# Kernel optimization log

Hardware: AMD Instinct MI355X
Metric: run time of the kernel (lower is better)

Reference implementation:

```python
import jax, jax.numpy as jnp
import numpy as np

N = 50000   # nodes
F = 128     # num_features (per branch)
E = 800000  # edges
G = 16      # graphs in batch
T = 3       # blocks per branch


def setup_inputs() -> dict:
    key = jax.random.key(0)
    ks = jax.random.split(key, 32)
    s = 0.05
    d = {}
    d["x"] = jax.random.normal(ks[0], (N, 2 * F), jnp.float32)
    d["edge_index"] = jax.random.randint(ks[1], (2, E), 0, N)
    d["edge_weight"] = jax.random.uniform(ks[2], (E,), jnp.float32)
    d["batch"] = jnp.sort(jax.random.randint(ks[3], (N,), 0, G))
    d["states"] = jax.random.randint(ks[4], (N,), 0, 2).astype(jnp.float32)

    def w(k, shape):
        return jax.random.normal(k, shape, jnp.float32) * s

    for i, p in enumerate(["p1", "p2"]):
        b = 5 + i * 5
        d[f"{p}_a0"] = w(ks[b], (T,))            # alpha0: Linear(1,1,bias=False) weight per block
        d[f"{p}_a1W"] = w(ks[b + 1], (T, F, F))    # alpha1 weight
        d[f"{p}_a1b"] = w(ks[b + 2], (T, F))       # alpha1 bias
        d[f"{p}_linW"] = w(ks[b + 3], (T, F, F))   # conv.lin weight
        d[f"{p}_linb"] = w(ks[b + 4], (T, F))      # conv.lin bias
    d["beta0_W"] = w(ks[15], (F, F))
    d["beta1_W"] = w(ks[16], (F, F))
    d["beta2_W"] = w(ks[17], (F, 2 * F))
    d["beta2_b"] = w(ks[18], (F,))
    d["gamma0_W"] = w(ks[19], (F, F))
    d["gamma1_W"] = w(ks[20], (F, F))
    d["gamma2_W"] = w(ks[21], (F, F))
    d["gamma3_W"] = w(ks[22], (3 * F // 2, 3 * F))
    d["gamma4_W"] = w(ks[23], (1, 3 * F // 2))
    d["gamma4_b"] = w(ks[24], (1,))
    return d


def _lrelu(v):
    return jax.nn.leaky_relu(v, 0.2)


def _block(x, states, a0, a1W, a1b, linW, linb, src, dst, ew):
    # x = lrelu(alpha1(x + alpha0(states)))
    h = _lrelu((x + states[:, None] * a0) @ a1W.T + a1b)
    # CustomGCNConv: lin then edge-weighted gather/scatter-add (source->target)
    h = h @ linW.T + linb
    msg = ew[:, None] * h[src]  # [E, F]
    return jax.ops.segment_sum(msg, dst, num_segments=x.shape[0])


def reference(x, edge_index, edge_weight, batch, states,
              p1_a0, p1_a1W, p1_a1b, p1_linW, p1_linb,
              p2_a0, p2_a1W, p2_a1b, p2_linW, p2_linb,
              beta0_W, beta1_W, beta2_W, beta2_b,
              gamma0_W, gamma1_W, gamma2_W, gamma3_W, gamma4_W, gamma4_b):
    Fh = x.shape[1] // 2
    x1, x2 = x[:, :Fh], x[:, Fh:]
    s0, s1 = edge_index[0], edge_index[1]
    x1s = jnp.zeros_like(x1)
    x2s = jnp.zeros_like(x2)
    for t in range(T):
        # branch1 uses reversed edges edge_index[[1,0]]
        x1 = _lrelu(_block(x1, states, p1_a0[t], p1_a1W[t], p1_a1b[t],
                           p1_linW[t], p1_linb[t], s1, s0, edge_weight))
        x2 = _lrelu(_block(x2, states, p2_a0[t], p2_a1W[t], p2_a1b[t],
                           p2_linW[t], p2_linb[t], s0, s1, edge_weight))
        x1s = x1s + x1
        x2s = x2s + x2
    xc = _lrelu(jnp.concatenate([x1s @ beta0_W.T, x2s @ beta1_W.T], -1) @ beta2_W.T + beta2_b)
    sel = (states == 1.0)[:, None]
    # per-graph pooled sums broadcast back to nodes (== repeat_interleave since batch is sorted)
    x_s = jax.ops.segment_sum(jnp.where(sel, xc, 0.0), batch, num_segments=G)[batch]
    x_sum = jax.ops.segment_sum(xc, batch, num_segments=G)[batch]
    h = jnp.concatenate([xc @ gamma0_W.T, x_s @ gamma1_W.T, x_sum @ gamma2_W.T], -1)
    h = _lrelu(h @ gamma3_W.T)
    return (h @ gamma4_W.T + gamma4_b).reshape(-1)
```

## Files before the change

kernel.cpp:

```cpp
#include <hip/hip_runtime.h>

typedef short s8v __attribute__((ext_vector_type(8)));
typedef float f32x4 __attribute__((ext_vector_type(4)));

#define LRELU(v) ((v) > 0.f ? (v) : 0.2f * (v))

constexpr int NBK = 391;
constexpr int TILE = 2048;
constexpr int CAP = 4096;

__device__ __forceinline__ float b2f(unsigned short b) {
  return __uint_as_float(((unsigned int)b) << 16);
}
__device__ __forceinline__ unsigned short f2b(float f) {
  unsigned int x = __float_as_uint(f);
  x += 0x7fffu + ((x >> 16) & 1u);
  return (unsigned short)(x >> 16);
}
__device__ __forceinline__ unsigned int pack2(float lo, float hi) {
  return ((unsigned int)f2b(hi) << 16) | (unsigned int)f2b(lo);
}

struct FArgs {
  const unsigned short* X[2];
  const unsigned short* W1[2];
  const float* b1[2];
  const float* a0p[2];
  const float* rowsum[2];
  const unsigned short* W2[2];
  const float* b2[2];
  unsigned short* H[2];
  const float* states;
  int N;
};

__global__ __launch_bounds__(256) void fused_mlp_kernel(FArgs fa)
{
  __shared__ __align__(16) unsigned short Ws[128 * 128];
  __shared__ __align__(16) unsigned short Tp[128 * 128];
  const int d = blockIdx.y;
  const int tid = threadIdx.x;
  const int lane = tid & 63;
  const int w = tid >> 6;
  const int l15 = lane & 15;
  const int g = lane >> 4;
  const int m0 = blockIdx.x * 128;
  const int N = fa.N;

#pragma unroll
  for (int j = 0; j < 8; ++j) {
    int idx = tid + j * 256;
    int o = idx >> 4, c = idx & 15;
    uint4 v = *(const uint4*)(fa.W1[d] + (size_t)o * 128 + c * 8);
    *(uint4*)&Ws[o * 128 + (c ^ (o & 15)) * 8] = v;
  }
  s8v a[2][4];
#pragma unroll
  for (int mf = 0; mf < 2; ++mf) {
    int row = m0 + w * 32 + mf * 16 + l15;
    const unsigned short* ar = fa.X[d] + (size_t)row * 128 + g * 8;
#pragma unroll
    for (int ks = 0; ks < 4; ++ks) {
      s8v t = {};
      if (row < N) t = *(const s8v*)(ar + ks * 32);
      a[mf][ks] = t;
    }
  }
  f32x4 zero4 = {0.f, 0.f, 0.f, 0.f};
  f32x4 acc[2][8];
#pragma unroll
  for (int mf = 0; mf < 2; ++mf)
#pragma unroll
    for (int nf = 0; nf < 8; ++nf) acc[mf][nf] = zero4;
  __syncthreads();
#pragma unroll
  for (int ks = 0; ks < 4; ++ks) {
#pragma unroll
    for (int nf = 0; nf < 8; ++nf) {
      int c = ks * 4 + g;
      s8v b = *(const s8v*)&Ws[(nf * 16 + l15) * 128 + (c ^ l15) * 8];
      acc[0][nf] = __builtin_amdgcn_mfma_f32_16x16x32_bf16(a[0][ks], b, acc[0][nf], 0, 0, 0);
      acc[1][nf] = __builtin_amdgcn_mfma_f32_16x16x32_bf16(a[1][ks], b, acc[1][nf], 0, 0, 0);
    }
  }
  const float a0 = fa.a0p[d][0];
#pragma unroll
  for (int mf = 0; mf < 2; ++mf) {
#pragma unroll
    for (int r = 0; r < 4; ++r) {
      int lrow = w * 32 + mf * 16 + g * 4 + r;
      int row = m0 + lrow;
      float sa = (row < N) ? fa.states[row] * a0 : 0.f;
#pragma unroll
      for (int nf = 0; nf < 8; ++nf) {
        int col = nf * 16 + l15;
        float v = 0.f;
        if (row < N) {
          v = acc[mf][nf][r] + fa.b1[d][col] + sa * fa.rowsum[d][col];
          v = LRELU(v);
        }
        int cch = col >> 3;
        Tp[lrow * 128 + ((cch ^ (lrow & 15)) << 3) + (col & 7)] = f2b(v);
      }
    }
  }
  __syncthreads();
#pragma unroll
  for (int j = 0; j < 8; ++j) {
    int idx = tid + j * 256;
    int o = idx >> 4, c = idx & 15;
    uint4 v = *(const uint4*)(fa.W2[d] + (size_t)o * 128 + c * 8);
    *(uint4*)&Ws[o * 128 + (c ^ (o & 15)) * 8] = v;
  }
  __syncthreads();
#pragma unroll
  for (int mf = 0; mf < 2; ++mf) {
    int lrow = w * 32 + mf * 16 + l15;
#pragma unroll
    for (int ks = 0; ks < 4; ++ks) {
      int c2 = ks * 4 + g;
      a[mf][ks] = *(const s8v*)&Tp[lrow * 128 + ((c2 ^ (lrow & 15)) << 3)];
    }
  }
#pragma unroll
  for (int mf = 0; mf < 2; ++mf)
#pragma unroll
    for (int nf = 0; nf < 8; ++nf) acc[mf][nf] = zero4;
#pragma unroll
  for (int ks = 0; ks < 4; ++ks) {
#pragma unroll
    for (int nf = 0; nf < 8; ++nf) {
      int c = ks * 4 + g;
      s8v b = *(const s8v*)&Ws[(nf * 16 + l15) * 128 + (c ^ l15) * 8];
      acc[0][nf] = __builtin_amdgcn_mfma_f32_16x16x32_bf16(a[0][ks], b, acc[0][nf], 0, 0, 0);
      acc[1][nf] = __builtin_amdgcn_mfma_f32_16x16x32_bf16(a[1][ks], b, acc[1][nf], 0, 0, 0);
    }
  }
#pragma unroll
  for (int mf = 0; mf < 2; ++mf) {
#pragma unroll
    for (int r = 0; r < 4; ++r) {
      int row = m0 + w * 32 + mf * 16 + g * 4 + r;
      if (row >= N) continue;
      unsigned short* crow = fa.H[d] + (size_t)row * 128;
#pragma unroll
      for (int nf = 0; nf < 8; ++nf) {
        int col = nf * 16 + l15;
        crow[col] = f2b(acc[mf][nf][r] + fa.b2[d][col]);
      }
    }
  }
}

struct PBArgs {
  const unsigned short* U[2];
  const unsigned short* Wb[2];
  const unsigned short* Wb2;
  const float* bias;
  unsigned short* XC;
  int N;
};

__global__ __launch_bounds__(256) void fused_beta_kernel(PBArgs pa)
{
  __shared__ __align__(16) unsigned short Ws[128 * 128];
  __shared__ __align__(16) unsigned short Tp[128 * 128];
  const int tid = threadIdx.x;
  const int lane = tid & 63;
  const int w = tid >> 6;
  const int l15 = lane & 15;
  const int g = lane >> 4;
  const int m0 = blockIdx.x * 128;
  const int N = pa.N;
  f32x4 zero4 = {0.f, 0.f, 0.f, 0.f};
  s8v a[2][4];
  f32x4 accf[2][8];
#pragma unroll
  for (int mf = 0; mf < 2; ++mf)
#pragma unroll
    for (int nf = 0; nf < 8; ++nf) accf[mf][nf] = zero4;

  for (int ph = 0; ph < 2; ++ph) {
#pragma unroll
    for (int j = 0; j < 8; ++j) {
      int idx = tid + j * 256;
      int o = idx >> 4, c = idx & 15;
      uint4 v = *(const uint4*)(pa.Wb[ph] + (size_t)o * 128 + c * 8);
      *(uint4*)&Ws[o * 128 + (c ^ (o & 15)) * 8] = v;
    }
#pragma unroll
    for (int mf = 0; mf < 2; ++mf) {
      int row = m0 + w * 32 + mf * 16 + l15;
      const unsigned short* ar = pa.U[ph] + (size_t)row * 128 + g * 8;
#pragma unroll
      for (int ks = 0; ks < 4; ++ks) {
        s8v t = {};
        if (row < N) t = *(const s8v*)(ar + ks * 32);
        a[mf][ks] = t;
      }
    }
    f32x4 acc[2][8];
#pragma unroll
    for (int mf = 0; mf < 2; ++mf)
#pragma unroll
      for (int nf = 0; nf < 8; ++nf) acc[mf][nf] = zero4;
    __syncthreads();
#pragma unroll
    for (int ks = 0; ks < 4; ++ks) {
#pragma unroll
      for (int nf = 0; nf < 8; ++nf) {
        int c = ks * 4 + g;
        s8v b = *(const s8v*)&Ws[(nf * 16 + l15) * 128 + (c ^ l15) * 8];
        acc[0][nf] = __builtin_amdgcn_mfma_f32_16x16x32_bf16(a[0][ks], b, acc[0][nf], 0, 0, 0);
        acc[1][nf] = __builtin_amdgcn_mfma_f32_16x16x32_bf16(a[1][ks], b, acc[1][nf], 0, 0, 0);
      }
    }
    __syncthreads();
#pragma unroll
    for (int mf = 0; mf < 2; ++mf) {
#pragma unroll
      for (int r = 0; r < 4; ++r) {
        int lrow = w * 32 + mf * 16 + g * 4 + r;
        int row = m0 + lrow;
#pragma unroll
        for (int nf = 0; nf < 8; ++nf) {
          int col = nf * 16 + l15;
          float v = (row < N) ? acc[mf][nf][r] : 0.f;
          int cch = col >> 3;
          Tp[lrow * 128 + ((cch ^ (lrow & 15)) << 3) + (col & 7)] = f2b(v);
        }
      }
    }
    __syncthreads();
#pragma unroll
    for (int j = 0; j < 8; ++j) {
      int idx = tid + j * 256;
      int o = idx >> 4, c = idx & 15;
      uint4 v = *(const uint4*)(pa.Wb2 + (size_t)o * 256 + ph * 128 + c * 8);
      *(uint4*)&Ws[o * 128 + (c ^ (o & 15)) * 8] = v;
    }
#pragma unroll
    for (int mf = 0; mf < 2; ++mf) {
      int lrow = w * 32 + mf * 16 + l15;
#pragma unroll
      for (int ks = 0; ks < 4; ++ks) {
        int c2 = ks * 4 + g;
        a[mf][ks] = *(const s8v*)&Tp[lrow * 128 + ((c2 ^ (lrow & 15)) << 3)];
      }
    }
    __syncthreads();
#pragma unroll
    for (int ks = 0; ks < 4; ++ks) {
#pragma unroll
      for (int nf = 0; nf < 8; ++nf) {
        int c = ks * 4 + g;
        s8v b = *(const s8v*)&Ws[(nf * 16 + l15) * 128 + (c ^ l15) * 8];
        accf[0][nf] = __builtin_amdgcn_mfma_f32_16x16x32_bf16(a[0][ks], b, accf[0][nf], 0, 0, 0);
        accf[1][nf] = __builtin_amdgcn_mfma_f32_16x16x32_bf16(a[1][ks], b, accf[1][nf], 0, 0, 0);
      }
    }
    __syncthreads();
  }
#pragma unroll
  for (int mf = 0; mf < 2; ++mf) {
#pragma unroll
    for (int r = 0; r < 4; ++r) {
      int row = m0 + w * 32 + mf * 16 + g * 4 + r;
      if (row >= N) continue;
      unsigned short* crow = pa.XC + (size_t)row * 128;
#pragma unroll
      for (int nf = 0; nf < 8; ++nf) {
        int col = nf * 16 + l15;
        float v = accf[mf][nf][r] + pa.bias[col];
        crow[col] = f2b(LRELU(v));
      }
    }
  }
}

__global__ __launch_bounds__(256) void g3_kernel(
    const unsigned short* __restrict__ xc,
    const unsigned short* __restrict__ A16,
    const unsigned short* __restrict__ B16,
    const int* __restrict__ batch,
    const unsigned short* __restrict__ W0,
    const unsigned short* __restrict__ W3,
    const float* __restrict__ g4W,
    const float* __restrict__ g4b,
    float* __restrict__ out, int N)
{
  constexpr int NF = 12;
  __shared__ __align__(16) unsigned short Ws[192 * 128];
  __shared__ __align__(16) unsigned short Tp[128 * 128];
  const int tid = threadIdx.x;
  const int lane = tid & 63;
  const int w = tid >> 6;
  const int l15 = lane & 15;
  const int g = lane >> 4;
  const int m0 = blockIdx.x * 128;

  f32x4 zero4 = {0.f, 0.f, 0.f, 0.f};
  s8v a[2][4];

#pragma unroll
  for (int j = 0; j < 8; ++j) {
    int idx = tid + j * 256;
    int o = idx >> 4, c = idx & 15;
    uint4 v = *(const uint4*)(W0 + (size_t)o * 128 + c * 8);
    *(uint4*)&Ws[o * 128 + (c ^ (o & 15)) * 8] = v;
  }
#pragma unroll
  for (int mf = 0; mf < 2; ++mf) {
    int row = m0 + w * 32 + mf * 16 + l15;
    const unsigned short* ar = xc + (size_t)row * 128 + g * 8;
#pragma unroll
    for (int ks = 0; ks < 4; ++ks) {
      s8v t = {};
      if (row < N) t = *(const s8v*)(ar + ks * 32);
      a[mf][ks] = t;
    }
  }
  {
    f32x4 acc1[2][8];
#pragma unroll
    for (int mf = 0; mf < 2; ++mf)
#pragma unroll
      for (int nf = 0; nf < 8; ++nf) acc1[mf][nf] = zero4;
    __syncthreads();
#pragma unroll
    for (int ks = 0; ks < 4; ++ks) {
#pragma unroll
      for (int nf = 0; nf < 8; ++nf) {
        int c = ks * 4 + g;
        s8v b = *(const s8v*)&Ws[(nf * 16 + l15) * 128 + (c ^ l15) * 8];
        acc1[0][nf] = __builtin_amdgcn_mfma_f32_16x16x32_bf16(a[0][ks], b, acc1[0][nf], 0, 0, 0);
        acc1[1][nf] = __builtin_amdgcn_mfma_f32_16x16x32_bf16(a[1][ks], b, acc1[1][nf], 0, 0, 0);
      }
    }
#pragma unroll
    for (int mf = 0; mf < 2; ++mf) {
#pragma unroll
      for (int r = 0; r < 4; ++r) {
        int lrow = w * 32 + mf * 16 + g * 4 + r;
        int row = m0 + lrow;
#pragma unroll
        for (int nf = 0; nf < 8; ++nf) {
          int col = nf * 16 + l15;
          float v = (row < N) ? acc1[mf][nf][r] : 0.f;
          int cch = col >> 3;
          Tp[lrow * 128 + ((cch ^ (lrow & 15)) << 3) + (col & 7)] = f2b(v);
        }
      }
    }
  }
  __syncthreads();

  f32x4 acc[2][NF];
#pragma unroll
  for (int mf = 0; mf < 2; ++mf)
#pragma unroll
    for (int nf = 0; nf < NF; ++nf) acc[mf][nf] = zero4;

  int brow[2];
#pragma unroll
  for (int mf = 0; mf < 2; ++mf) {
    int row = m0 + w * 32 + mf * 16 + l15;
    brow[mf] = (row < N) ? batch[row] : 0;
  }

  for (int kk = 0; kk < 384; kk += 128) {
#pragma unroll
    for (int j = 0; j < NF; ++j) {
      int idx = tid + j * 256;
      int o = idx >> 4, c = idx & 15;
      uint4 v = *(const uint4*)(W3 + (size_t)o * 384 + kk + c * 8);
      *(uint4*)&Ws[o * 128 + (c ^ (o & 15)) * 8] = v;
    }
    if (kk == 0) {
#pragma unroll
      for (int mf = 0; mf < 2; ++mf) {
        int lrow = w * 32 + mf * 16 + l15;
#pragma unroll
        for (int ks = 0; ks < 4; ++ks) {
          int c2 = ks * 4 + g;
          a[mf][ks] = *(const s8v*)&Tp[lrow * 128 + ((c2 ^ (lrow & 15)) << 3)];
        }
      }
    } else {
#pragma unroll
      for (int mf = 0; mf < 2; ++mf) {
        int row = m0 + w * 32 + mf * 16 + l15;
        const unsigned short* ar = ((kk == 128) ? A16 : B16) + (size_t)brow[mf] * 128 + g * 8;
#pragma unroll
        for (int ks = 0; ks < 4; ++ks) {
          s8v t = {};
          if (row < N) t = *(const s8v*)(ar + ks * 32);
          a[mf][ks] = t;
        }
      }
    }
    __syncthreads();
#pragma unroll
    for (int ks = 0; ks < 4; ++ks) {
#pragma unroll
      for (int nf = 0; nf < NF; ++nf) {
        int c = ks * 4 + g;
        s8v b = *(const s8v*)&Ws[(nf * 16 + l15) * 128 + (c ^ l15) * 8];
        acc[0][nf] = __builtin_amdgcn_mfma_f32_16x16x32_bf16(a[0][ks], b, acc[0][nf], 0, 0, 0);
        acc[1][nf] = __builtin_amdgcn_mfma_f32_16x16x32_bf16(a[1][ks], b, acc[1][nf], 0, 0, 0);
      }
    }
    if (kk < 256) __syncthreads();
  }

  float w4[NF];
#pragma unroll
  for (int nf = 0; nf < NF; ++nf) w4[nf] = g4W[nf * 16 + l15];
  const float gb = g4b[0];

#pragma unroll
  for (int mf = 0; mf < 2; ++mf) {
#pragma unroll
    for (int r = 0; r < 4; ++r) {
      int row = m0 + w * 32 + mf * 16 + g * 4 + r;
      float dot = 0.f;
#pragma unroll
      for (int nf = 0; nf < NF; ++nf) {
        float v = acc[mf][nf][r];
        v = LRELU(v);
        dot += v * w4[nf];
      }
#pragma unroll
      for (int m = 1; m < 16; m <<= 1) dot += __shfl_xor(dot, m, 16);
      if (l15 == 0 && row < N) out[row] = dot + gb;
    }
  }
}

struct CJobs { const float* s[9]; unsigned short* d[9]; int n[9]; };
__global__ void convert_kernel(CJobs jb) {
  int j = blockIdx.y;
  int idx = (blockIdx.x * 256 + threadIdx.x) * 8;
  if (idx >= jb.n[j]) return;
  const float* s = jb.s[j] + idx;
  float4 p0 = *(const float4*)s;
  float4 p1 = *(const float4*)(s + 4);
  uint4 u;
  u.x = pack2(p0.x, p0.y); u.y = pack2(p0.z, p0.w);
  u.z = pack2(p1.x, p1.y); u.w = pack2(p1.z, p1.w);
  *(uint4*)(jb.d[j] + idx) = u;
}

__global__ void rowsum_kernel(const float* __restrict__ a1,
                              const float* __restrict__ a2, float* __restrict__ rs) {
  int j = blockIdx.x;
  const float* src = (j < 3) ? (a1 + (size_t)j * 16384) : (a2 + (size_t)(j - 3) * 16384);
  int o = threadIdx.x;
  float s = 0.f;
  for (int k = 0; k < 128; ++k) s += src[o * 128 + k];
  rs[j * 128 + o] = s;
}

__global__ void init_kernel(const float* __restrict__ x,
                            unsigned short* __restrict__ x1, unsigned short* __restrict__ x2,
                            int n)
{
  int idx = blockIdx.x * blockDim.x + threadIdx.x;
  int total = n * 16;
  for (; idx < total; idx += gridDim.x * blockDim.x) {
    int r = idx >> 4, c = idx & 15;
    const float* xr = x + (size_t)r * 256 + c * 8;
    float4 p0 = *(const float4*)xr;
    float4 p1 = *(const float4*)(xr + 4);
    uint4 u1;
    u1.x = pack2(p0.x, p0.y); u1.y = pack2(p0.z, p0.w);
    u1.z = pack2(p1.x, p1.y); u1.w = pack2(p1.z, p1.w);
    float4 q0 = *(const float4*)(xr + 128);
    float4 q1 = *(const float4*)(xr + 132);
    uint4 u2;
    u2.x = pack2(q0.x, q0.y); u2.y = pack2(q0.z, q0.w);
    u2.z = pack2(q1.x, q1.y); u2.w = pack2(q1.z, q1.w);
    ((uint4*)(x1 + (size_t)r * 128))[c] = u1;
    ((uint4*)(x2 + (size_t)r * 128))[c] = u2;
  }
}

struct BinArgs {
  const int* s0; const int* s1; const float* ew;
  int* bcur0; int* bcur1;
  unsigned long long* bin0; unsigned long long* bin1;
  int E;
};
__global__ __launch_bounds__(256) void bin_kernel(BinArgs ba)
{
  __shared__ int hist0[NBK], hist1[NBK];
  __shared__ int base0[NBK], base1[NBK];
  const int t = threadIdx.x;
  const int e0 = blockIdx.x * TILE;
  const int e1 = min(e0 + TILE, ba.E);
  for (int i = t; i < NBK; i += 256) { hist0[i] = 0; hist1[i] = 0; }
  __syncthreads();
  for (int e = e0 + t; e < e1; e += 256) {
    atomicAdd(&hist0[ba.s0[e] >> 7], 1);
    atomicAdd(&hist1[ba.s1[e] >> 7], 1);
  }
  __syncthreads();
  for (int i = t; i < NBK; i += 256) {
    int c0 = hist0[i];
    base0[i] = c0 ? atomicAdd(&ba.bcur0[i], c0) : 0;
    int c1 = hist1[i];
    base1[i] = c1 ? atomicAdd(&ba.bcur1[i], c1) : 0;
  }
  __syncthreads();
  for (int i = t; i < NBK; i += 256) { hist0[i] = 0; hist1[i] = 0; }
  __syncthreads();
  for (int e = e0 + t; e < e1; e += 256) {
    int d0 = ba.s0[e], d1 = ba.s1[e];
    unsigned long long wb = (unsigned long long)__float_as_uint(ba.ew[e]) << 32;
    int b0 = d0 >> 7, b1 = d1 >> 7;
    int r0 = base0[b0] + atomicAdd(&hist0[b0], 1);
    if (r0 < CAP)
      ba.bin0[(size_t)b0 * CAP + r0] = wb | (unsigned int)((d0 & 127) << 16) | (unsigned int)d1;
    int r1 = base1[b1] + atomicAdd(&hist1[b1], 1);
    if (r1 < CAP)
      ba.bin1[(size_t)b1 * CAP + r1] = wb | (unsigned int)((d1 & 127) << 16) | (unsigned int)d0;
  }
}

struct BScanArgs { const int* cnt[2]; int* bbase[2]; float* gsel; float* gsum; };
__global__ __launch_bounds__(128) void bscan_kernel(BScanArgs a)
{
  __shared__ int ld[2][NBK];
  int wid = threadIdx.x >> 6, lane = threadIdx.x & 63;
  for (int i = threadIdx.x; i < 2048; i += 128) { a.gsel[i] = 0.f; a.gsum[i] = 0.f; }
  for (int i = lane; i < NBK; i += 64) ld[wid][i] = a.cnt[wid][i];
  __syncthreads();
  if (lane == 0) {
    int acc = 0;
    for (int i = 0; i < NBK; ++i) { int v = ld[wid][i]; ld[wid][i] = acc; acc += v; }
    a.bbase[wid][NBK] = acc;
  }
  __syncthreads();
  for (int i = lane; i < NBK; i += 64) a.bbase[wid][i] = ld[wid][i];
}

struct RArgs {
  const int* bbase[2];
  const unsigned long long* bin[2];
  unsigned int* comb[2];
  int* row[2];
  int n;
};
__global__ __launch_bounds__(256) void reorder_kernel(RArgs ra)
{
  const int d = blockIdx.y;
  const int b = blockIdx.x;
  const unsigned long long* __restrict__ bin = ra.bin[d] + (size_t)b * CAP;
  unsigned int* __restrict__ comb = ra.comb[d];
  int* __restrict__ row = ra.row[d];
  const int nb = b * 128;
  const int ne = min(nb + 128, ra.n);
  const int t = threadIdx.x;
  __shared__ int lcnt[128];
  __shared__ int lcur[128];
  __shared__ int wtot[4];
  if (t < 128) lcnt[t] = 0;
  const int span_beg = ra.bbase[d][b];
  const int span_end = ra.bbase[d][b + 1];
  const int cnt = span_end - span_beg;
  __syncthreads();
  for (int i = t; i < cnt; i += 256) {
    int nl = ((unsigned int)bin[i] >> 16) & 127;
    atomicAdd(&lcnt[nl], 1);
  }
  __syncthreads();
  int lane = t & 63, wv = t >> 6;
  int v = (t < 128) ? lcnt[t] : 0;
  int sc = v;
#pragma unroll
  for (int off = 1; off < 64; off <<= 1) {
    int u = __shfl_up(sc, off, 64);
    if (lane >= off) sc += u;
  }
  if (lane == 63) wtot[wv] = sc;
  __syncthreads();
  int excl = sc - v + ((wv == 1) ? wtot[0] : 0);
  if (t < 128) {
    lcur[t] = excl;
    if (nb + t < ne) row[nb + t] = span_beg + excl;
  }
  if (b == NBK - 1 && t == 0) row[ra.n] = span_end;
  __syncthreads();
  for (int i = t; i < cnt; i += 256) {
    unsigned long long r = bin[i];
    unsigned int lo = (unsigned int)r;
    float w = __uint_as_float((unsigned int)(r >> 32));
    int nl = (lo >> 16) & 127;
    int slot = atomicAdd(&lcur[nl], 1);
    comb[span_beg + slot] = (lo & 0xffffu) | ((unsigned int)f2b(w) << 16);
  }
}

struct GArgs {
  const int* rowstart[2];
  const unsigned int* comb[2];
  const unsigned short* h[2];
  unsigned short* xout[2];
  const unsigned int* add1[2];
  const unsigned int* add2[2];
  int n;
};
__global__ void gather_kernel(GArgs ga)
{
  int quad = blockIdx.x * (blockDim.x >> 6) + (threadIdx.x >> 6);
  int lane = threadIdx.x & 63;
  int sub = lane >> 4;
  int fl = lane & 15;
  long long gnode = (long long)4 * quad + sub;
  bool valid = gnode < 2 * ga.n;
  int dir = (valid && gnode >= ga.n) ? 1 : 0;
  int node = valid ? (int)(gnode - (long long)dir * ga.n) : 0;
  const int* __restrict__ rowstart = ga.rowstart[dir];
  const unsigned int* __restrict__ comb = ga.comb[dir];
  const unsigned int* __restrict__ h = (const unsigned int*)ga.h[dir];
  int beg = rowstart[node], end = rowstart[node + 1];
  if (!valid) end = beg;
  int nch_own = (end - beg + 7) >> 3;
  int m1 = max(nch_own, __shfl_xor(nch_own, 16, 64));
  int nch = max(m1, __shfl_xor(m1, 32, 64));
  float a0 = 0.f, a1 = 0.f, a2 = 0.f, a3 = 0.f;
  float a4 = 0.f, a5 = 0.f, a6 = 0.f, a7 = 0.f;
  for (int ch = 0; ch < nch; ++ch) {
    int p0 = beg + ch * 8;
    unsigned int cc[8];
    uint4 uu[8];
#pragma unroll
    for (int i = 0; i < 8; ++i) {
      int pi = p0 + i;
      cc[i] = (pi < end) ? comb[pi] : 0u;
    }
#pragma unroll
    for (int i = 0; i < 8; ++i)
      uu[i] = *(const uint4*)(h + (size_t)(cc[i] & 0xffffu) * 64 + fl * 4);
#pragma unroll
    for (int i = 0; i < 8; ++i) {
      float wv = b2f((unsigned short)(cc[i] >> 16));
      a0 += wv * b2f((unsigned short)uu[i].x);
      a1 += wv * b2f((unsigned short)(uu[i].x >> 16));
      a2 += wv * b2f((unsigned short)uu[i].y);
      a3 += wv * b2f((unsigned short)(uu[i].y >> 16));
      a4 += wv * b2f((unsigned short)uu[i].z);
      a5 += wv * b2f((unsigned short)(uu[i].z >> 16));
      a6 += wv * b2f((unsigned short)uu[i].w);
      a7 += wv * b2f((unsigned short)(uu[i].w >> 16));
    }
  }
  float v0 = LRELU(a0), v1 = LRELU(a1), v2 = LRELU(a2), v3 = LRELU(a3);
  float v4 = LRELU(a4), v5 = LRELU(a5), v6 = LRELU(a6), v7 = LRELU(a7);
  if (ga.add1[0]) {
    uint4 ua = ((const uint4*)ga.add1[dir])[(size_t)node * 16 + fl];
    uint4 ub = ((const uint4*)ga.add2[dir])[(size_t)node * 16 + fl];
    v0 += b2f((unsigned short)ua.x) + b2f((unsigned short)ub.x);
    v1 += b2f((unsigned short)(ua.x >> 16)) + b2f((unsigned short)(ub.x >> 16));
    v2 += b2f((unsigned short)ua.y) + b2f((unsigned short)ub.y);
    v3 += b2f((unsigned short)(ua.y >> 16)) + b2f((unsigned short)(ub.y >> 16));
    v4 += b2f((unsigned short)ua.z) + b2f((unsigned short)ub.z);
    v5 += b2f((unsigned short)(ua.z >> 16)) + b2f((unsigned short)(ub.z >> 16));
    v6 += b2f((unsigned short)ua.w) + b2f((unsigned short)ub.w);
    v7 += b2f((unsigned short)(ua.w >> 16)) + b2f((unsigned short)(ub.w >> 16));
  }
  if (valid) {
    uint4 o;
    o.x = pack2(v0, v1);
    o.y = pack2(v2, v3);
    o.z = pack2(v4, v5);
    o.w = pack2(v6, v7);
    ((uint4*)(ga.xout[dir] + (size_t)node * 128))[fl] = o;
  }
}

__global__ __launch_bounds__(256) void segsum_kernel(
    const unsigned short* __restrict__ xc, const int* __restrict__ batch,
    const float* __restrict__ states,
    float* __restrict__ gsel, float* __restrict__ gsum, int n)
{
  int slot = threadIdx.x >> 6;
  int lane = threadIdx.x & 63;
  int r0 = blockIdx.x * 128 + slot * 32;
  if (r0 >= n) return;
  int r1 = min(r0 + 32, n);
  const unsigned int* __restrict__ xcu = (const unsigned int*)xc;
  float sel0 = 0.f, sel1 = 0.f, sum0 = 0.f, sum1 = 0.f;
  int cur = batch[r0];
  for (int r = r0; r < r1; r += 4) {
    unsigned int u[4]; int bb[4]; float st[4];
#pragma unroll
    for (int i = 0; i < 4; ++i) {
      int ri = min(r + i, r1 - 1);
      u[i] = xcu[(size_t)ri * 64 + lane];
      bb[i] = batch[ri];
      st[i] = states[ri];
    }
    int m = min(4, r1 - r);
#pragma unroll
    for (int i = 0; i < 4; ++i) {
      if (i >= m) break;
      if (bb[i] != cur) {
        atomicAdd(&gsel[cur * 128 + lane * 2], sel0);
        atomicAdd(&gsel[cur * 128 + lane * 2 + 1], sel1);
        atomicAdd(&gsum[cur * 128 + lane * 2], sum0);
        atomicAdd(&gsum[cur * 128 + lane * 2 + 1], sum1);
        sel0 = sel1 = sum0 = sum1 = 0.f;
        cur = bb[i];
      }
      float lo = b2f((unsigned short)u[i]);
      float hi = b2f((unsigned short)(u[i] >> 16));
      sum0 += lo; sum1 += hi;
      if (st[i] == 1.0f) { sel0 += lo; sel1 += hi; }
    }
  }
  atomicAdd(&gsel[cur * 128 + lane * 2], sel0);
  atomicAdd(&gsel[cur * 128 + lane * 2 + 1], sel1);
  atomicAdd(&gsum[cur * 128 + lane * 2], sum0);
  atomicAdd(&gsum[cur * 128 + lane * 2 + 1], sum1);
}

__global__ void small16_kernel(const float* __restrict__ gsel, const float* __restrict__ gsum,
                               const float* __restrict__ g1W, const float* __restrict__ g2W,
                               unsigned short* __restrict__ A16, unsigned short* __restrict__ B16)
{
  int r = blockIdx.x, t = threadIdx.x, o = t & 127;
  const float* src = (t < 128) ? gsel : gsum;
  const float* Wm  = (t < 128) ? g1W : g2W;
  float acc = 0.f;
  for (int k = 0; k < 128; ++k) acc += src[r * 128 + k] * Wm[o * 128 + k];
  unsigned short* dst = (t < 128) ? A16 : B16;
  dst[r * 128 + o] = f2b(acc);
}

extern "C" void kernel_launch(void* const* d_in, const int* in_sizes, int n_in,
                              void* d_out, int out_size, void* d_ws, size_t ws_size,
                              hipStream_t stream)
{
  const int N = 50000, F = 128, E = 800000, G = 16, T = 3;
  const float* x      = (const float*)d_in[0];
  const int*   ei     = (const int*)d_in[1];
  const int*   s0     = ei;
  const int*   s1     = ei + E;
  const float* ew     = (const float*)d_in[2];
  const int*   batch  = (const int*)d_in[3];
  const float* states = (const float*)d_in[4];
  const float* p_a0[2]   = {(const float*)d_in[5],  (const float*)d_in[10]};
  const float* p_a1W[2]  = {(const float*)d_in[6],  (const float*)d_in[11]};
  const float* p_a1b[2]  = {(const float*)d_in[7],  (const float*)d_in[12]};
  const float* p_linW[2] = {(const float*)d_in[8],  (const float*)d_in[13]};
  const float* p_linb[2] = {(const float*)d_in[9],  (const float*)d_in[14]};
  const float* beta0W = (const float*)d_in[15];
  const float* beta1W = (const float*)d_in[16];
  const float* beta2W = (const float*)d_in[17];
  const float* beta2b = (const float*)d_in[18];
  const float* g0W = (const float*)d_in[19];
  const float* g1W = (const float*)d_in[20];
  const float* g2W = (const float*)d_in[21];
  const float* g3W = (const float*)d_in[22];
  const float* g4W = (const float*)d_in[23];
  const float* g4b = (const float*)d_in[24];
  float* out = (float*)d_out;

  char* p = (char*)d_ws;
  auto alloc = [&](size_t bytes) {
    char* r = p;
    p += (bytes + 255) & ~(size_t)255;
    return r;
  };
  const size_t NFb2 = (size_t)N * F * sizeof(unsigned short);
  unsigned short* X1[3] = {(unsigned short*)alloc(NFb2), (unsigned short*)alloc(NFb2),
                           (unsigned short*)alloc(NFb2)};
  unsigned short* X2[3] = {(unsigned short*)alloc(NFb2), (unsigned short*)alloc(NFb2),
                           (unsigned short*)alloc(NFb2)};
  unsigned short* TMP0 = (unsigned short*)alloc(NFb2);
  unsigned short* TMP1 = (unsigned short*)alloc(NFb2);
  unsigned short* HH0  = (unsigned short*)alloc(NFb2);
  unsigned short* HH1  = (unsigned short*)alloc(NFb2);
  int*   row0 = (int*)alloc((size_t)(N + 1) * 4);
  int*   row1 = (int*)alloc((size_t)(N + 1) * 4);
  int*   bbase0 = (int*)alloc((size_t)(NBK + 1) * 4);
  int*   bbase1 = (int*)alloc((size_t)(NBK + 1) * 4);
  int*   bcur0 = (int*)alloc((size_t)NBK * 4);
  int*   bcur1 = (int*)alloc((size_t)NBK * 4);
  unsigned long long* bin0 = (unsigned long long*)alloc((size_t)NBK * CAP * 8);
  unsigned long long* bin1 = (unsigned long long*)alloc((size_t)NBK * CAP * 8);
  unsigned int* comb0 = (unsigned int*)alloc((size_t)E * 4);
  unsigned int* comb1 = (unsigned int*)alloc((size_t)E * 4);
  float* gsel = (float*)alloc((size_t)G * F * 4);
  float* gsum = (float*)alloc((size_t)G * F * 4);
  unsigned short* A16b = (unsigned short*)alloc((size_t)G * F * 2);
  unsigned short* B16b = (unsigned short*)alloc((size_t)G * F * 2);
  unsigned short* wreg = (unsigned short*)alloc((size_t)352256 * 2);
  float* rs = (float*)alloc((size_t)6 * 128 * 4);

  unsigned short* a1Wb[2]  = {wreg + 0,      wreg + 49152};
  unsigned short* linWb[2] = {wreg + 98304,  wreg + 147456};
  unsigned short* b0b = wreg + 196608;
  unsigned short* b1b = wreg + 212992;
  unsigned short* b2b = wreg + 229376;
  unsigned short* g0b = wreg + 262144;
  unsigned short* g3b = wreg + 278528;

  const dim3 blk256(256);
  const int GX = (N + 127) / 128;
  const int EB = (E + TILE - 1) / TILE;

  hipMemsetAsync(bcur0, 0, (size_t)NBK * 4, stream);
  hipMemsetAsync(bcur1, 0, (size_t)NBK * 4, stream);
  BinArgs bna;
  bna.s0 = s0; bna.s1 = s1; bna.ew = ew;
  bna.bcur0 = bcur0; bna.bcur1 = bcur1;
  bna.bin0 = bin0; bna.bin1 = bin1;
  bna.E = E;
  bin_kernel<<<EB, blk256, 0, stream>>>(bna);
  BScanArgs bsa;
  bsa.cnt[0] = bcur0; bsa.cnt[1] = bcur1;
  bsa.bbase[0] = bbase0; bsa.bbase[1] = bbase1;
  bsa.gsel = gsel; bsa.gsum = gsum;
  bscan_kernel<<<1, 128, 0, stream>>>(bsa);
  RArgs ra;
  ra.bbase[0] = bbase0; ra.bbase[1] = bbase1;
  ra.bin[0] = bin0; ra.bin[1] = bin1;
  ra.comb[0] = comb0; ra.comb[1] = comb1;
  ra.row[0] = row0; ra.row[1] = row1;
  ra.n = N;
  reorder_kernel<<<dim3(NBK, 2), blk256, 0, stream>>>(ra);

  CJobs jb;
  jb.s[0] = p_a1W[0];  jb.d[0] = a1Wb[0];  jb.n[0] = 49152;
  jb.s[1] = p_a1W[1];  jb.d[1] = a1Wb[1];  jb.n[1] = 49152;
  jb.s[2] = p_linW[0]; jb.d[2] = linWb[0]; jb.n[2] = 49152;
  jb.s[3] = p_linW[1]; jb.d[3] = linWb[1]; jb.n[3] = 49152;
  jb.s[4] = beta0W;    jb.d[4] = b0b;      jb.n[4] = 16384;
  jb.s[5] = beta1W;    jb.d[5] = b1b;      jb.n[5] = 16384;
  jb.s[6] = beta2W;    jb.d[6] = b2b;      jb.n[6] = 32768;
  jb.s[7] = g0W;       jb.d[7] = g0b;      jb.n[7] = 16384;
  jb.s[8] = g3W;       jb.d[8] = g3b;      jb.n[8] = 73728;
  convert_kernel<<<dim3(36, 9), blk256, 0, stream>>>(jb);
  rowsum_kernel<<<6, 128, 0, stream>>>(p_a1W[0], p_a1W[1], rs);
  init_kernel<<<3125, blk256, 0, stream>>>(x, X1[0], X2[0], N);

  for (int t = 0; t < T; ++t) {
    int rv = t % 3, wv = (t + 1) % 3;

    FArgs fa;
    fa.X[0] = X1[rv];  fa.X[1] = X2[rv];
    fa.W1[0] = a1Wb[0] + t * 16384;  fa.W1[1] = a1Wb[1] + t * 16384;
    fa.b1[0] = p_a1b[0] + t * F;     fa.b1[1] = p_a1b[1] + t * F;
    fa.a0p[0] = p_a0[0] + t;         fa.a0p[1] = p_a0[1] + t;
    fa.rowsum[0] = rs + t * 128;     fa.rowsum[1] = rs + (3 + t) * 128;
    fa.W2[0] = linWb[0] + t * 16384; fa.W2[1] = linWb[1] + t * 16384;
    fa.b2[0] = p_linb[0] + t * F;    fa.b2[1] = p_linb[1] + t * F;
    fa.H[0] = HH0;  fa.H[1] = HH1;
    fa.states = states;  fa.N = N;
    fused_mlp_kernel<<<dim3(GX, 2), blk256, 0, stream>>>(fa);

    GArgs ga;
    ga.rowstart[0] = row0; ga.rowstart[1] = row1;
    ga.comb[0] = comb0;    ga.comb[1] = comb1;
    ga.h[0] = HH0;         ga.h[1] = HH1;
    if (t == T - 1) {
      ga.xout[0] = TMP0;  ga.xout[1] = TMP1;
      ga.add1[0] = (const unsigned int*)X1[1];  ga.add1[1] = (const unsigned int*)X2[1];
      ga.add2[0] = (const unsigned int*)X1[2];  ga.add2[1] = (const unsigned int*)X2[2];
    } else {
      ga.xout[0] = X1[wv];  ga.xout[1] = X2[wv];
      ga.add1[0] = nullptr; ga.add1[1] = nullptr;
      ga.add2[0] = nullptr; ga.add2[1] = nullptr;
    }
    ga.n = N;
    gather_kernel<<<(2 * N + 15) / 16, blk256, 0, stream>>>(ga);
  }

  PBArgs pb;
  pb.U[0] = TMP0; pb.U[1] = TMP1;
  pb.Wb[0] = b0b; pb.Wb[1] = b1b; pb.Wb2 = b2b;
  pb.bias = beta2b; pb.XC = HH0; pb.N = N;
  fused_beta_kernel<<<GX, blk256, 0, stream>>>(pb);

  segsum_kernel<<<GX, blk256, 0, stream>>>(HH0, batch, states, gsel, gsum, N);
  small16_kernel<<<G, blk256, 0, stream>>>(gsel, gsum, g1W, g2W, A16b, B16b);

  g3_kernel<<<GX, blk256, 0, stream>>>(HH0, A16b, B16b, batch, g0b, g3b, g4W, g4b, out, N);
}
```

Measured before the change: 421.7 us.

## Merge preamble kernels and vectorize gather edge loads with nontemporal hints

Folds the feature conversion, weight conversion, rowsum and bin-counter memsets into one preamble kernel, replacing three kernel launches and two memset calls with a single launch. In the gather kernel, edge chunks are now aligned down to multiples of 8 and loaded as two 16-byte nontemporal vector loads, with out-of-range entries masked by zeroing their weight. Residual loads and the output store also become nontemporal. The aligned loads read a few neighbouring edges' entries and can run past the array end at the final chunk. The preamble must also finish before bin_kernel uses the zeroed counters, which stream order guarantees.

Result: slower. 482.2 us (+14.3%).

```diff
diff --git a/kernel.cpp b/kernel.cpp
--- a/kernel.cpp
+++ b/kernel.cpp
@@ -2,6 +2,7 @@
 
 typedef short s8v __attribute__((ext_vector_type(8)));
 typedef float f32x4 __attribute__((ext_vector_type(4)));
+typedef unsigned int u32x4 __attribute__((ext_vector_type(4)));
 
 #define LRELU(v) ((v) > 0.f ? (v) : 0.2f * (v))
 
@@ -437,51 +438,65 @@
   }
 }
 
-struct CJobs { const float* s[9]; unsigned short* d[9]; int n[9]; };
-__global__ void convert_kernel(CJobs jb) {
-  int j = blockIdx.y;
-  int idx = (blockIdx.x * 256 + threadIdx.x) * 8;
-  if (idx >= jb.n[j]) return;
-  const float* s = jb.s[j] + idx;
-  float4 p0 = *(const float4*)s;
-  float4 p1 = *(const float4*)(s + 4);
-  uint4 u;
-  u.x = pack2(p0.x, p0.y); u.y = pack2(p0.z, p0.w);
-  u.z = pack2(p1.x, p1.y); u.w = pack2(p1.z, p1.w);
-  *(uint4*)(jb.d[j] + idx) = u;
-}
-
-__global__ void rowsum_kernel(const float* __restrict__ a1,
-                              const float* __restrict__ a2, float* __restrict__ rs) {
-  int j = blockIdx.x;
-  const float* src = (j < 3) ? (a1 + (size_t)j * 16384) : (a2 + (size_t)(j - 3) * 16384);
-  int o = threadIdx.x;
-  float s = 0.f;
-  for (int k = 0; k < 128; ++k) s += src[o * 128 + k];
-  rs[j * 128 + o] = s;
-}
-
-__global__ void init_kernel(const float* __restrict__ x,
-                            unsigned short* __restrict__ x1, unsigned short* __restrict__ x2,
-                            int n)
-{
-  int idx = blockIdx.x * blockDim.x + threadIdx.x;
-  int total = n * 16;
-  for (; idx < total; idx += gridDim.x * blockDim.x) {
-    int r = idx >> 4, c = idx & 15;
-    const float* xr = x + (size_t)r * 256 + c * 8;
-    float4 p0 = *(const float4*)xr;
-    float4 p1 = *(const float4*)(xr + 4);
-    uint4 u1;
-    u1.x = pack2(p0.x, p0.y); u1.y = pack2(p0.z, p0.w);
-    u1.z = pack2(p1.x, p1.y); u1.w = pack2(p1.z, p1.w);
-    float4 q0 = *(const float4*)(xr + 128);
-    float4 q1 = *(const float4*)(xr + 132);
-    uint4 u2;
-    u2.x = pack2(q0.x, q0.y); u2.y = pack2(q0.z, q0.w);
-    u2.z = pack2(q1.x, q1.y); u2.w = pack2(q1.z, q1.w);
-    ((uint4*)(x1 + (size_t)r * 128))[c] = u1;
-    ((uint4*)(x2 + (size_t)r * 128))[c] = u2;
+struct PreArgs {
+  const float* src[9];
+  unsigned short* wreg;
+  int cum[10];
+  const float* a1; const float* a2; float* rs;
+  const float* x;
+  unsigned short* x1; unsigned short* x2;
+  int* bcur0; int* bcur1;
+  int n;
+};
+
+__global__ __launch_bounds__(256) void preamble_kernel(PreArgs pa)
+{
+  const int NINIT = 3125;
+  const int NCONV = 172;
+  int b = blockIdx.x;
+  int t = threadIdx.x;
+  if (b < NINIT) {
+    int idx = b * 256 + t;
+    if (idx < pa.n * 16) {
+      int r = idx >> 4, c = idx & 15;
+      const float* xr = pa.x + (size_t)r * 256 + c * 8;
+      float4 p0 = *(const float4*)xr;
+      float4 p1 = *(const float4*)(xr + 4);
+      uint4 u1;
+      u1.x = pack2(p0.x, p0.y); u1.y = pack2(p0.z, p0.w);
+      u1.z = pack2(p1.x, p1.y); u1.w = pack2(p1.z, p1.w);
+      float4 q0 = *(const float4*)(xr + 128);
+      float4 q1 = *(const float4*)(xr + 132);
+      uint4 u2;
+      u2.x = pack2(q0.x, q0.y); u2.y = pack2(q0.z, q0.w);
+      u2.z = pack2(q1.x, q1.y); u2.w = pack2(q1.z, q1.w);
+      ((uint4*)(pa.x1 + (size_t)r * 128))[c] = u1;
+      ((uint4*)(pa.x2 + (size_t)r * 128))[c] = u2;
+    }
+  } else if (b < NINIT + NCONV) {
+    int e = ((b - NINIT) * 256 + t) * 8;
+    if (e < pa.cum[9]) {
+      int j = 0;
+#pragma unroll
+      for (int k = 1; k < 9; ++k) if (e >= pa.cum[k]) j = k;
+      const float* s = pa.src[j] + (e - pa.cum[j]);
+      float4 p0 = *(const float4*)s;
+      float4 p1 = *(const float4*)(s + 4);
+      uint4 u;
+      u.x = pack2(p0.x, p0.y); u.y = pack2(p0.z, p0.w);
+      u.z = pack2(p1.x, p1.y); u.w = pack2(p1.z, p1.w);
+      *(uint4*)(pa.wreg + e) = u;
+    }
+  } else if (b < NINIT + NCONV + 6) {
+    int j = b - NINIT - NCONV;
+    if (t < 128) {
+      const float* src = (j < 3) ? (pa.a1 + (size_t)j * 16384) : (pa.a2 + (size_t)(j - 3) * 16384);
+      float s = 0.f;
+      for (int k = 0; k < 128; ++k) s += src[t * 128 + k];
+      pa.rs[j * 128 + t] = s;
+    }
+  } else {
+    for (int i = t; i < NBK; i += 256) { pa.bcur0[i] = 0; pa.bcur1[i] = 0; }
   }
 }
 
@@ -624,27 +639,29 @@
   const unsigned int* __restrict__ comb = ga.comb[dir];
   const unsigned int* __restrict__ h = (const unsigned int*)ga.h[dir];
   int beg = rowstart[node], end = rowstart[node + 1];
-  if (!valid) end = beg;
-  int nch_own = (end - beg + 7) >> 3;
+  if (!valid) { beg = 0; end = 0; }
+  int pstart = beg & ~7;
+  int nch_own = (end - pstart + 7) >> 3;
+  if (end <= pstart) nch_own = 0;
   int m1 = max(nch_own, __shfl_xor(nch_own, 16, 64));
   int nch = max(m1, __shfl_xor(m1, 32, 64));
   float a0 = 0.f, a1 = 0.f, a2 = 0.f, a3 = 0.f;
   float a4 = 0.f, a5 = 0.f, a6 = 0.f, a7 = 0.f;
   for (int ch = 0; ch < nch; ++ch) {
-    int p0 = beg + ch * 8;
+    int p0 = pstart + ch * 8;
+    u32x4 ca = __builtin_nontemporal_load((const u32x4*)(comb + p0));
+    u32x4 cb = __builtin_nontemporal_load((const u32x4*)(comb + p0 + 4));
     unsigned int cc[8];
+    cc[0] = ca.x; cc[1] = ca.y; cc[2] = ca.z; cc[3] = ca.w;
+    cc[4] = cb.x; cc[5] = cb.y; cc[6] = cb.z; cc[7] = cb.w;
     uint4 uu[8];
+#pragma unroll
+    for (int i = 0; i < 8; ++i)
+      uu[i] = *(const uint4*)(h + (size_t)(cc[i] & 0xffffu) * 64 + fl * 4);
 #pragma unroll
     for (int i = 0; i < 8; ++i) {
       int pi = p0 + i;
-      cc[i] = (pi < end) ? comb[pi] : 0u;
-    }
-#pragma unroll
-    for (int i = 0; i < 8; ++i)
-      uu[i] = *(const uint4*)(h + (size_t)(cc[i] & 0xffffu) * 64 + fl * 4);
-#pragma unroll
-    for (int i = 0; i < 8; ++i) {
-      float wv = b2f((unsigned short)(cc[i] >> 16));
+      float wv = (pi >= beg && pi < end) ? b2f((unsigned short)(cc[i] >> 16)) : 0.f;
       a0 += wv * b2f((unsigned short)uu[i].x);
       a1 += wv * b2f((unsigned short)(uu[i].x >> 16));
       a2 += wv * b2f((unsigned short)uu[i].y);
@@ -658,8 +675,8 @@
   float v0 = LRELU(a0), v1 = LRELU(a1), v2 = LRELU(a2), v3 = LRELU(a3);
   float v4 = LRELU(a4), v5 = LRELU(a5), v6 = LRELU(a6), v7 = LRELU(a7);
   if (ga.add1[0]) {
-    uint4 ua = ((const uint4*)ga.add1[dir])[(size_t)node * 16 + fl];
-    uint4 ub = ((const uint4*)ga.add2[dir])[(size_t)node * 16 + fl];
+    u32x4 ua = __builtin_nontemporal_load((const u32x4*)ga.add1[dir] + (size_t)node * 16 + fl);
+    u32x4 ub = __builtin_nontemporal_load((const u32x4*)ga.add2[dir] + (size_t)node * 16 + fl);
     v0 += b2f((unsigned short)ua.x) + b2f((unsigned short)ub.x);
     v1 += b2f((unsigned short)(ua.x >> 16)) + b2f((unsigned short)(ub.x >> 16));
     v2 += b2f((unsigned short)ua.y) + b2f((unsigned short)ub.y);
@@ -670,12 +687,12 @@
     v7 += b2f((unsigned short)(ua.w >> 16)) + b2f((unsigned short)(ub.w >> 16));
   }
   if (valid) {
-    uint4 o;
+    u32x4 o;
     o.x = pack2(v0, v1);
     o.y = pack2(v2, v3);
     o.z = pack2(v4, v5);
     o.w = pack2(v6, v7);
-    ((uint4*)(ga.xout[dir] + (size_t)node * 128))[fl] = o;
+    __builtin_nontemporal_store(o, (u32x4*)(ga.xout[dir] + (size_t)node * 128) + fl);
   }
 }
 
@@ -811,8 +828,20 @@
   const int GX = (N + 127) / 128;
   const int EB = (E + TILE - 1) / TILE;
 
-  hipMemsetAsync(bcur0, 0, (size_t)NBK * 4, stream);
-  hipMemsetAsync(bcur1, 0, (size_t)NBK * 4, stream);
+  PreArgs pra;
+  pra.src[0] = p_a1W[0];  pra.src[1] = p_a1W[1];
+  pra.src[2] = p_linW[0]; pra.src[3] = p_linW[1];
+  pra.src[4] = beta0W;    pra.src[5] = beta1W;  pra.src[6] = beta2W;
+  pra.src[7] = g0W;       pra.src[8] = g3W;
+  pra.wreg = wreg;
+  int cums[10] = {0, 49152, 98304, 147456, 196608, 212992, 229376, 262144, 278528, 352256};
+  for (int i = 0; i < 10; ++i) pra.cum[i] = cums[i];
+  pra.a1 = p_a1W[0]; pra.a2 = p_a1W[1]; pra.rs = rs;
+  pra.x = x; pra.x1 = X1[0]; pra.x2 = X2[0];
+  pra.bcur0 = bcur0; pra.bcur1 = bcur1;
+  pra.n = N;
+  preamble_kernel<<<3125 + 172 + 6 + 1, blk256, 0, stream>>>(pra);
+
   BinArgs bna;
   bna.s0 = s0; bna.s1 = s1; bna.ew = ew;
   bna.bcur0 = bcur0; bna.bcur1 = bcur1;
@@ -832,20 +861,6 @@
   ra.n = N;
   reorder_kernel<<<dim3(NBK, 2), blk256, 0, stream>>>(ra);
 
-  CJobs jb;
-  jb.s[0] = p_a1W[0];  jb.d[0] = a1Wb[0];  jb.n[0] = 49152;
-  jb.s[1] = p_a1W[1];  jb.d[1] = a1Wb[1];  jb.n[1] = 49152;
-  jb.s[2] = p_linW[0]; jb.d[2] = linWb[0]; jb.n[2] = 49152;
-  jb.s[3] = p_linW[1]; jb.d[3] = linWb[1]; jb.n[3] = 49152;
-  jb.s[4] = beta0W;    jb.d[4] = b0b;      jb.n[4] = 16384;
-  jb.s[5] = beta1W;    jb.d[5] = b1b;      jb.n[5] = 16384;
-  jb.s[6] = beta2W;    jb.d[6] = b2b;      jb.n[6] = 32768;
-  jb.s[7] = g0W;       jb.d[7] = g0b;      jb.n[7] = 16384;
-  jb.s[8] = g3W;       jb.d[8] = g3b;      jb.n[8] = 73728;
-  convert_kernel<<<dim3(36, 9), blk256, 0, stream>>>(jb);
-  rowsum_kernel<<<6, 128, 0, stream>>>(p_a1W[0], p_a1W[1], rs);
-  init_kernel<<<3125, blk256, 0, stream>>>(x, X1[0], X2[0], N);
-
   for (int t = 0; t < T; ++t) {
     int rv = t % 3, wv = (t + 1) % 3;
 
```
